# Performance work log

Measured on AMD Instinct MI355X. Metric: run time of the kernel, lower is better.

The kernel has to match this reference:

```python
import jax, jax.numpy as jnp
import numpy as np

B, C_IN, T = 8, 1024, 4096
D_VQ, K, DS = 1024, 2048, 2


def setup_inputs() -> dict:
    key = jax.random.key(0)
    k1, k2, k3, k4 = jax.random.split(key, 4)
    x = jax.random.normal(k1, (B, C_IN, T), dtype=jnp.float32)
    x_mask = jnp.ones((B, 1, T), dtype=jnp.float32)
    conv_in_w = jax.random.normal(k2, (D_VQ, C_IN, DS), dtype=jnp.float32) * 0.02
    conv_in_b = jnp.zeros((D_VQ,), dtype=jnp.float32)
    codebook = jax.random.normal(k3, (K, D_VQ), dtype=jnp.float32)
    conv_out_w = jax.random.normal(k4, (C_IN, D_VQ), dtype=jnp.float32) * 0.02
    conv_out_b = jnp.zeros((C_IN,), dtype=jnp.float32)
    return {"x": x, "x_mask": x_mask, "conv_in_w": conv_in_w,
            "conv_in_b": conv_in_b, "codebook": codebook,
            "conv_out_w": conv_out_w, "conv_out_b": conv_out_b}


def reference(x, x_mask, conv_in_w, conv_in_b, codebook, conv_out_w, conv_out_b):
    x_len = x.shape[2]  # 4096, divisible by DS=2 -> no padding branch
    # conv_in: Conv1d(C_IN -> D_VQ, kernel=DS, stride=DS)
    h = jax.lax.conv_general_dilated(
        x, conv_in_w, window_strides=(DS,), padding='VALID',
        dimension_numbers=('NCH', 'OIH', 'NCH')) + conv_in_b[None, :, None]
    xt = h.transpose(0, 2, 1)  # [B, T', D]
    # euclidean VQ: squared distances to codebook, argmin assignment
    d2 = (jnp.sum(xt * xt, -1, keepdims=True)
          - 2.0 * jnp.einsum('btd,kd->btk', xt, codebook)
          + jnp.sum(codebook * codebook, -1))  # [B, T', K]
    idx = jnp.argmin(d2, axis=-1)  # [B, T'] int
    quant = codebook[idx]  # [B, T', D]
    # commitment loss (EMA codebook: codebook detached)
    loss = jnp.mean(jnp.square(xt - jax.lax.stop_gradient(quant)))
    # straight-through estimator
    q = xt + jax.lax.stop_gradient(quant - xt)
    qc = q.transpose(0, 2, 1)  # [B, D, T']
    # conv_out: nearest upsample by DS, then 1x1 conv
    up = jnp.repeat(qc, DS, axis=-1)  # [B, D, T]
    out = jnp.einsum('od,bdt->bot', conv_out_w, up) + conv_out_b[None, :, None]
    out = (out * x_mask)[:, :, :x_len]
    indices = idx[:, None, :]  # 'b t -> b 1 t'
    return out, indices, loss
```

## Files before the change

kernel.cpp:

```cpp
#include <hip/hip_runtime.h>

#define NB   8
#define CIN  1024
#define TT   4096
#define DVQ  1024
#define KC   2048
#define MM   16384

typedef short s16x8 __attribute__((ext_vector_type(8)));
typedef float f32x4 __attribute__((ext_vector_type(4)));

__device__ __forceinline__ short f2bf(float f) {
    unsigned u = __float_as_uint(f);
    u = u + 0x7fffu + ((u >> 16) & 1u);
    return (short)(u >> 16);
}
__device__ __forceinline__ float bf2f(short h) {
    return __uint_as_float(((unsigned)(unsigned short)h) << 16);
}
__device__ __forceinline__ unsigned pk(short a, short b) {
    return (unsigned)(unsigned short)a | ((unsigned)(unsigned short)b << 16);
}
__device__ __forceinline__ void split3(float v, short& h, short& m, short& l) {
    h = f2bf(v); float r1 = v - bf2f(h);
    m = f2bf(r1); float r2 = r1 - bf2f(m);
    l = f2bf(r2);
}
__device__ __forceinline__ int aswz(int row, int q) {
    return row * 40 + (((q ^ (row >> 3)) & 3) << 3);
}
__device__ __forceinline__ bool lesskey(float v, int k, float v2, int k2) {
    return v < v2 || (v == v2 && k < k2);
}
__device__ __forceinline__ void merge2(float& b1, int& k1, float& b2, int& k2,
                                       float o1, int ok1, float o2, int ok2) {
    if (lesskey(o1, ok1, b1, k1)) {
        float nb2; int nk2;
        if (lesskey(b1, k1, o2, ok2)) { nb2 = b1; nk2 = k1; } else { nb2 = o2; nk2 = ok2; }
        b1 = o1; k1 = ok1; b2 = nb2; k2 = nk2;
    } else if (lesskey(o1, ok1, b2, k2)) {
        b2 = o1; k2 = ok1;
    }
}
__device__ __forceinline__ void gload16(void* lds, const void* g) {
    __builtin_amdgcn_global_load_lds((const __attribute__((address_space(1))) void*)g,
                                     (__attribute__((address_space(3))) void*)lds, 16, 0, 0);
}

__global__ __launch_bounds__(256) void k_split3(const float* __restrict__ src,
                                                short* __restrict__ h, short* __restrict__ m,
                                                short* __restrict__ l, int n4) {
    int i = blockIdx.x * 256 + threadIdx.x;
    if (i >= n4) return;
    float4 v = ((const float4*)src)[i];
    short4 H, M, L;
    split3(v.x, H.x, M.x, L.x); split3(v.y, H.y, M.y, L.y);
    split3(v.z, H.z, M.z, L.z); split3(v.w, H.w, M.w, L.w);
    ((short4*)h)[i] = H; ((short4*)m)[i] = M; ((short4*)l)[i] = L;
}

__global__ __launch_bounds__(256) void k_split2(const float* __restrict__ src,
                                                short* __restrict__ h, short* __restrict__ l, int n4) {
    int i = blockIdx.x * 256 + threadIdx.x;
    if (i >= n4) return;
    float4 v = ((const float4*)src)[i];
    short4 H, L;
    H.x = f2bf(v.x); L.x = f2bf(v.x - bf2f(H.x));
    H.y = f2bf(v.y); L.y = f2bf(v.y - bf2f(H.y));
    H.z = f2bf(v.z); L.z = f2bf(v.z - bf2f(H.z));
    H.w = f2bf(v.w); L.w = f2bf(v.w - bf2f(H.w));
    ((short4*)h)[i] = H; ((short4*)l)[i] = L;
}

__global__ __launch_bounds__(256) void k_cnorm(const float* __restrict__ cb,
                                               float* __restrict__ c32,
                                               double* __restrict__ c64) {
    __shared__ double red[256];
    const float* row = cb + (size_t)blockIdx.x * DVQ;
    float4 v = ((const float4*)row)[threadIdx.x];
    red[threadIdx.x] = (double)v.x * v.x + (double)v.y * v.y +
                       (double)v.z * v.z + (double)v.w * v.w;
    __syncthreads();
    for (int o = 128; o > 0; o >>= 1) {
        if (threadIdx.x < o) red[threadIdx.x] += red[threadIdx.x + o];
        __syncthreads();
    }
    if (threadIdx.x == 0) { c64[blockIdx.x] = red[0]; c32[blockIdx.x] = (float)red[0]; }
}

__global__ __launch_bounds__(256) void k_asplit(const float* __restrict__ x,
                                                short* __restrict__ ah,
                                                short* __restrict__ am,
                                                short* __restrict__ al) {
    const int bid = blockIdx.x;
    const int b = bid >> 7, cblk = (bid >> 5) & 3, tch = bid & 31;
    const int c = cblk * 256 + threadIdx.x;
    const float* xr = x + ((size_t)b * CIN + c) * TT + tch * 128;
    unsigned* AH = (unsigned*)ah;
    unsigned* AM = (unsigned*)am;
    unsigned* AL = (unsigned*)al;
    const int mbase = b * 2048 + tch * 64;
#pragma unroll 4
    for (int i = 0; i < 32; ++i) {
        float4 v = *(const float4*)(xr + 4 * i);
        short h0, mm0, l0, h1, mm1, l1, h2, mm2, l2, h3, mm3, l3;
        split3(v.x, h0, mm0, l0); split3(v.y, h1, mm1, l1);
        split3(v.z, h2, mm2, l2); split3(v.w, h3, mm3, l3);
        const size_t o0 = (size_t)(mbase + 2 * i) * 1024 + c;
        const size_t o1 = o0 + 1024;
        AH[o0] = pk(h0, h1); AM[o0] = pk(mm0, mm1); AL[o0] = pk(l0, l1);
        AH[o1] = pk(h2, h3); AM[o1] = pk(mm2, mm3); AL[o1] = pk(l2, l3);
    }
}

__global__ __launch_bounds__(512, 2) void k_convp(const short* __restrict__ ah,
                                                  const short* __restrict__ am,
                                                  const short* __restrict__ al,
                                                  const short* __restrict__ wh,
                                                  const short* __restrict__ wm,
                                                  const short* __restrict__ wl,
                                                  const float* __restrict__ bias,
                                                  float* __restrict__ xt,
                                                  short* __restrict__ xth,
                                                  short* __restrict__ xtl) {
    __shared__ short sA[2][3][256 * 32];
    __shared__ short sB[2][3][128 * 32];
    const int tid = threadIdx.x;
    const int lin = blockIdx.x;
    const int cx = lin & 7, j = lin >> 3;
    const int m0 = (cx * 8 + (j >> 3)) * 256;
    const int n0 = (j & 7) * 128;

    const int s0 = tid, s1 = tid + 512;
    const int ar0 = s0 >> 2, ac0 = ((s0 & 3) ^ ((s0 >> 3) & 3)) << 3;
    const int ar1 = s1 >> 2, ac1 = ((s1 & 3) ^ ((s1 >> 3) & 3)) << 3;
    const size_t gA0 = (size_t)(m0 + ar0) * 2048 + ac0;
    const size_t gA1 = (size_t)(m0 + ar1) * 2048 + ac1;
    const size_t gB0 = (size_t)(n0 + ar0) * 2048 + ac0;

    const int ln = tid & 15, quad = (tid >> 4) & 3, wv = tid >> 6;
    const int qsw = (quad ^ ((ln >> 1) & 3)) * 8;
    const int r0w = (wv >> 1) * 64, c0w = (wv & 1) * 64;

    f32x4 acc[4][4], sums[4][4];
#pragma unroll
    for (int r = 0; r < 4; ++r)
#pragma unroll
        for (int c = 0; c < 4; ++c) { acc[r][c] = 0.f; sums[r][c] = 0.f; }

#define STAGE(BUF, K0)                                        \
    do {                                                      \
        gload16(&sA[BUF][0][s0 * 8], ah + gA0 + (K0));        \
        gload16(&sA[BUF][0][s1 * 8], ah + gA1 + (K0));        \
        gload16(&sA[BUF][1][s0 * 8], am + gA0 + (K0));        \
        gload16(&sA[BUF][1][s1 * 8], am + gA1 + (K0));        \
        gload16(&sA[BUF][2][s0 * 8], al + gA0 + (K0));        \
        gload16(&sA[BUF][2][s1 * 8], al + gA1 + (K0));        \
        gload16(&sB[BUF][0][s0 * 8], wh + gB0 + (K0));        \
        gload16(&sB[BUF][1][s0 * 8], wm + gB0 + (K0));        \
        gload16(&sB[BUF][2][s0 * 8], wl + gB0 + (K0));        \
    } while (0)

    STAGE(0, 0);
    __syncthreads();

#pragma unroll 2
    for (int it = 0; it < 64; ++it) {
        const int cur = it & 1;
        if (it + 1 < 64) STAGE(cur ^ 1, (it + 1) * 32);

        s16x8 fa0[4], fa1[4], fa2[4];
#pragma unroll
        for (int r = 0; r < 4; ++r) {
            const int off = (r0w + r * 16 + ln) * 32 + qsw;
            fa0[r] = *(const s16x8*)&sA[cur][0][off];
            fa1[r] = *(const s16x8*)&sA[cur][1][off];
            fa2[r] = *(const s16x8*)&sA[cur][2][off];
        }
#pragma unroll
        for (int c = 0; c < 4; ++c) {
            const int boff = (c0w + c * 16 + ln) * 32 + qsw;
            s16x8 fbh = *(const s16x8*)&sB[cur][0][boff];
            s16x8 fbm = *(const s16x8*)&sB[cur][1][boff];
            s16x8 fbl = *(const s16x8*)&sB[cur][2][boff];
#pragma unroll
            for (int r = 0; r < 4; ++r) {
                acc[r][c] = __builtin_amdgcn_mfma_f32_16x16x32_bf16(fa0[r], fbh, acc[r][c], 0, 0, 0);
                acc[r][c] = __builtin_amdgcn_mfma_f32_16x16x32_bf16(fa0[r], fbm, acc[r][c], 0, 0, 0);
                acc[r][c] = __builtin_amdgcn_mfma_f32_16x16x32_bf16(fa1[r], fbh, acc[r][c], 0, 0, 0);
                acc[r][c] = __builtin_amdgcn_mfma_f32_16x16x32_bf16(fa0[r], fbl, acc[r][c], 0, 0, 0);
                acc[r][c] = __builtin_amdgcn_mfma_f32_16x16x32_bf16(fa1[r], fbm, acc[r][c], 0, 0, 0);
                acc[r][c] = __builtin_amdgcn_mfma_f32_16x16x32_bf16(fa2[r], fbh, acc[r][c], 0, 0, 0);
            }
        }
        if (it & 1) {
#pragma unroll
            for (int r = 0; r < 4; ++r)
#pragma unroll
                for (int c = 0; c < 4; ++c) { sums[r][c] += acc[r][c]; acc[r][c] = 0.f; }
        }
        __syncthreads();
    }
#undef STAGE
#pragma unroll
    for (int c = 0; c < 4; ++c) {
        const int n = n0 + c0w + c * 16 + ln;
        const float bv = bias[n];
#pragma unroll
        for (int r = 0; r < 4; ++r)
#pragma unroll
            for (int g = 0; g < 4; ++g) {
                const int m = m0 + r0w + r * 16 + quad * 4 + g;
                const float v = sums[r][c][g] + bv;
                const size_t o = (size_t)m * DVQ + n;
                xt[o] = v;
                short h = f2bf(v);
                xth[o] = h;
                xtl[o] = f2bf(v - bf2f(h));
            }
    }
}

__global__ __launch_bounds__(256, 2) void k_conv(const float* __restrict__ x,
                                                 const short* __restrict__ wh,
                                                 const short* __restrict__ wm,
                                                 const short* __restrict__ wl,
                                                 const float* __restrict__ bias,
                                                 float* __restrict__ xt,
                                                 short* __restrict__ xth,
                                                 short* __restrict__ xtl) {
    __shared__ short sAh[128 * 40], sAm[128 * 40], sAl[128 * 40];
    __shared__ short sBh[64 * 40],  sBm[64 * 40],  sBl[64 * 40];
    const int tid = threadIdx.x;
    const int lin = blockIdx.x;
    const int cx = lin & 7, j = lin >> 3;
    const int m0 = (cx * 16 + (j >> 4)) * 128;
    const int n0 = (j & 15) * 64;
    const int b = m0 >> 11, t0 = m0 & 2047;
    const float* xb = x + (size_t)b * CIN * TT + 2 * t0;

    const int aw = tid >> 6, p = tid & 63;
    const int brow = tid >> 2, bq = tid & 3;
    const int ln = tid & 15, quad = (tid >> 4) & 3;
    const int r0 = (aw >> 1) * 64, c0 = (aw & 1) * 32;

    f32x4 acc[4][2], sums[4][2];
#pragma unroll
    for (int r = 0; r < 4; ++r)
#pragma unroll
        for (int c = 0; c < 2; ++c) { acc[r][c] = 0.f; sums[r][c] = 0.f; }

    float4 av[4];
    uint4 bh0, bm0, bl0;
#pragma unroll
    for (int r = 0; r < 4; ++r) av[r] = *(const float4*)(xb + (size_t)(4 * r + aw) * TT + 4 * p);
    {
        const size_t o = (size_t)(n0 + brow) * 2048 + bq * 8;
        bh0 = *(const uint4*)&wh[o]; bm0 = *(const uint4*)&wm[o]; bl0 = *(const uint4*)&wl[o];
    }

    for (int it = 0; it < 64; ++it) {
        __syncthreads();
#pragma unroll
        for (int r = 0; r < 4; ++r) {
            const int ii = r * 4 + aw;
            const int q = ii >> 2, off = (2 * ii) & 7;
            const int a0 = aswz(2 * p, q) + off;
            const int a1 = aswz(2 * p + 1, q) + off;
            float4 v = av[r];
            short hx, mx, lx, hy, my, ly;
            split3(v.x, hx, mx, lx); split3(v.y, hy, my, ly);
            *(unsigned*)&sAh[a0] = pk(hx, hy);
            *(unsigned*)&sAm[a0] = pk(mx, my);
            *(unsigned*)&sAl[a0] = pk(lx, ly);
            split3(v.z, hx, mx, lx); split3(v.w, hy, my, ly);
            *(unsigned*)&sAh[a1] = pk(hx, hy);
            *(unsigned*)&sAm[a1] = pk(mx, my);
            *(unsigned*)&sAl[a1] = pk(lx, ly);
        }
        {
            const int w0 = brow * 40 + bq * 8;
            *(uint4*)&sBh[w0] = bh0; *(uint4*)&sBm[w0] = bm0; *(uint4*)&sBl[w0] = bl0;
        }
        __syncthreads();
        if (it + 1 < 64) {
            const int i0 = (it + 1) * 16, k0 = (it + 1) * 32;
#pragma unroll
            for (int r = 0; r < 4; ++r)
                av[r] = *(const float4*)(xb + (size_t)(i0 + 4 * r + aw) * TT + 4 * p);
            const size_t o = (size_t)(n0 + brow) * 2048 + k0 + bq * 8;
            bh0 = *(const uint4*)&wh[o]; bm0 = *(const uint4*)&wm[o]; bl0 = *(const uint4*)&wl[o];
        }
        s16x8 fah[4], fam[4], fal[4];
#pragma unroll
        for (int r = 0; r < 4; ++r) {
            const int base = aswz(r0 + r * 16 + ln, quad);
            fah[r] = *(const s16x8*)&sAh[base];
            fam[r] = *(const s16x8*)&sAm[base];
            fal[r] = *(const s16x8*)&sAl[base];
        }
#pragma unroll
        for (int c = 0; c < 2; ++c) {
            const int bb = (c0 + c * 16 + ln) * 40 + quad * 8;
            s16x8 fbh = *(const s16x8*)&sBh[bb];
            s16x8 fbm = *(const s16x8*)&sBm[bb];
            s16x8 fbl = *(const s16x8*)&sBl[bb];
#pragma unroll
            for (int r = 0; r < 4; ++r) {
                acc[r][c] = __builtin_amdgcn_mfma_f32_16x16x32_bf16(fah[r], fbh, acc[r][c], 0, 0, 0);
                acc[r][c] = __builtin_amdgcn_mfma_f32_16x16x32_bf16(fah[r], fbm, acc[r][c], 0, 0, 0);
                acc[r][c] = __builtin_amdgcn_mfma_f32_16x16x32_bf16(fam[r], fbh, acc[r][c], 0, 0, 0);
                acc[r][c] = __builtin_amdgcn_mfma_f32_16x16x32_bf16(fah[r], fbl, acc[r][c], 0, 0, 0);
                acc[r][c] = __builtin_amdgcn_mfma_f32_16x16x32_bf16(fam[r], fbm, acc[r][c], 0, 0, 0);
                acc[r][c] = __builtin_amdgcn_mfma_f32_16x16x32_bf16(fal[r], fbh, acc[r][c], 0, 0, 0);
            }
        }
        if (it & 1) {
#pragma unroll
            for (int r = 0; r < 4; ++r)
#pragma unroll
                for (int c = 0; c < 2; ++c) { sums[r][c] += acc[r][c]; acc[r][c] = 0.f; }
        }
    }
#pragma unroll
    for (int c = 0; c < 2; ++c) {
        const int n = n0 + c0 + c * 16 + ln;
        const float bv = bias[n];
#pragma unroll
        for (int r = 0; r < 4; ++r)
#pragma unroll
            for (int g = 0; g < 4; ++g) {
                const int m = m0 + r0 + r * 16 + quad * 4 + g;
                const float v = sums[r][c][g] + bv;
                const size_t o = (size_t)m * DVQ + n;
                xt[o] = v;
                short h = f2bf(v);
                xth[o] = h;
                xtl[o] = f2bf(v - bf2f(h));
            }
    }
}

__global__ __launch_bounds__(256, 2) void k_dot(const short* __restrict__ xth,
                                                const short* __restrict__ xtl,
                                                const short* __restrict__ cbh,
                                                const short* __restrict__ cbl,
                                                const float* __restrict__ c32,
                                                float4* __restrict__ pb) {
    __shared__ __align__(16) short sAh[128 * 40], sAl[128 * 40], sBh[128 * 40], sBl[128 * 40];
    const int tid = threadIdx.x;
    const int n0 = blockIdx.x * 128, m0 = blockIdx.y * 128;
    const int ar = tid >> 2, q = tid & 3, kk = q * 8;
    const int ln = tid & 15, quad = (tid >> 4) & 3, wv = tid >> 6;
    const int r0 = (wv >> 1) * 64, c0 = (wv & 1) * 64;

    f32x4 acc[4][4];
#pragma unroll
    for (int r = 0; r < 4; ++r)
#pragma unroll
        for (int c = 0; c < 4; ++c) acc[r][c] = 0.f;

    uint4 a0 = *(const uint4*)&xth[(size_t)(m0 + ar) * 1024 + kk];
    uint4 a1 = *(const uint4*)&xth[(size_t)(m0 + 64 + ar) * 1024 + kk];
    uint4 a2 = *(const uint4*)&xtl[(size_t)(m0 + ar) * 1024 + kk];
    uint4 a3 = *(const uint4*)&xtl[(size_t)(m0 + 64 + ar) * 1024 + kk];
    uint4 b0 = *(const uint4*)&cbh[(size_t)(n0 + ar) * 1024 + kk];
    uint4 b1 = *(const uint4*)&cbh[(size_t)(n0 + 64 + ar) * 1024 + kk];
    uint4 b2 = *(const uint4*)&cbl[(size_t)(n0 + ar) * 1024 + kk];
    uint4 b3 = *(const uint4*)&cbl[(size_t)(n0 + 64 + ar) * 1024 + kk];

    for (int it = 0; it < 32; ++it) {
        __syncthreads();
        *(uint4*)&sAh[aswz(ar, q)] = a0;
        *(uint4*)&sAh[aswz(64 + ar, q)] = a1;
        *(uint4*)&sAl[aswz(ar, q)] = a2;
        *(uint4*)&sAl[aswz(64 + ar, q)] = a3;
        {
            const int w0 = ar * 40 + kk, w1 = (64 + ar) * 40 + kk;
            *(uint4*)&sBh[w0] = b0; *(uint4*)&sBh[w1] = b1;
            *(uint4*)&sBl[w0] = b2; *(uint4*)&sBl[w1] = b3;
        }
        __syncthreads();
        if (it + 1 < 32) {
            const int k0 = (it + 1) * 32;
            a0 = *(const uint4*)&xth[(size_t)(m0 + ar) * 1024 + k0 + kk];
            a1 = *(const uint4*)&xth[(size_t)(m0 + 64 + ar) * 1024 + k0 + kk];
            a2 = *(const uint4*)&xtl[(size_t)(m0 + ar) * 1024 + k0 + kk];
            a3 = *(const uint4*)&xtl[(size_t)(m0 + 64 + ar) * 1024 + k0 + kk];
            b0 = *(const uint4*)&cbh[(size_t)(n0 + ar) * 1024 + k0 + kk];
            b1 = *(const uint4*)&cbh[(size_t)(n0 + 64 + ar) * 1024 + k0 + kk];
            b2 = *(const uint4*)&cbl[(size_t)(n0 + ar) * 1024 + k0 + kk];
            b3 = *(const uint4*)&cbl[(size_t)(n0 + 64 + ar) * 1024 + k0 + kk];
        }
        s16x8 fah[4], fal[4];
#pragma unroll
        for (int r = 0; r < 4; ++r) {
            const int base = aswz(r0 + r * 16 + ln, quad);
            fah[r] = *(const s16x8*)&sAh[base];
            fal[r] = *(const s16x8*)&sAl[base];
        }
#pragma unroll
        for (int c = 0; c < 4; ++c) {
            const int bb = (c0 + c * 16 + ln) * 40 + quad * 8;
            s16x8 fbh = *(const s16x8*)&sBh[bb];
            s16x8 fbl = *(const s16x8*)&sBl[bb];
#pragma unroll
            for (int r = 0; r < 4; ++r) {
                acc[r][c] = __builtin_amdgcn_mfma_f32_16x16x32_bf16(fah[r], fbh, acc[r][c], 0, 0, 0);
                acc[r][c] = __builtin_amdgcn_mfma_f32_16x16x32_bf16(fah[r], fbl, acc[r][c], 0, 0, 0);
                acc[r][c] = __builtin_amdgcn_mfma_f32_16x16x32_bf16(fal[r], fbh, acc[r][c], 0, 0, 0);
            }
        }
    }
    float tb1[16], tb2[16]; int tk1[16], tk2[16];
#pragma unroll
    for (int i = 0; i < 16; ++i) { tb1[i] = INFINITY; tb2[i] = INFINITY; tk1[i] = 0; tk2[i] = 0; }
#pragma unroll
    for (int c = 0; c < 4; ++c) {
        const int n = n0 + c0 + c * 16 + ln;
        const float cn = c32[n];
#pragma unroll
        for (int r = 0; r < 4; ++r)
#pragma unroll
            for (int g = 0; g < 4; ++g) {
                const float s = cn - 2.0f * acc[r][c][g];
                const int i = r * 4 + g;
                if (s < tb1[i]) { tb2[i] = tb1[i]; tk2[i] = tk1[i]; tb1[i] = s; tk1[i] = n; }
                else if (s < tb2[i]) { tb2[i] = s; tk2[i] = n; }
            }
    }
#pragma unroll
    for (int off = 1; off < 16; off <<= 1) {
#pragma unroll
        for (int i = 0; i < 16; ++i) {
            float o1 = __shfl_xor(tb1[i], off); int ok1 = __shfl_xor(tk1[i], off);
            float o2 = __shfl_xor(tb2[i], off); int ok2 = __shfl_xor(tk2[i], off);
            merge2(tb1[i], tk1[i], tb2[i], tk2[i], o1, ok1, o2, ok2);
        }
    }
    __syncthreads();
    float4* part = (float4*)sAh;
    if (ln == 0) {
#pragma unroll
        for (int i = 0; i < 16; ++i) {
            const int lr = (i >> 2) * 16 + quad * 4 + (i & 3);
            float4 v; v.x = tb1[i]; v.y = tb2[i];
            v.z = __int_as_float(tk1[i]); v.w = __int_as_float(tk2[i]);
            part[wv * 64 + lr] = v;
        }
    }
    __syncthreads();
    if (tid < 128) {
        const int row = tid, h = row >> 6, lr = row & 63;
        float4 A = part[(2 * h) * 64 + lr];
        float4 B = part[(2 * h + 1) * 64 + lr];
        float b1v = A.x, b2v = A.y; int k1 = __float_as_int(A.z), k2 = __float_as_int(A.w);
        merge2(b1v, k1, b2v, k2, B.x, __float_as_int(B.z), B.y, __float_as_int(B.w));
        float4 o; o.x = b1v; o.y = b2v; o.z = __int_as_float(k1); o.w = __int_as_float(k2);
        pb[(size_t)blockIdx.x * MM + m0 + row] = o;
    }
}

__global__ __launch_bounds__(256) void k_pick(const float4* __restrict__ pb,
                                              const double* __restrict__ c64,
                                              const float* __restrict__ xt,
                                              const float* __restrict__ cb,
                                              int* __restrict__ idxbuf,
                                              float* __restrict__ idx_out) {
    const int wv = threadIdx.x >> 6, lane = threadIdx.x & 63;
    const int m = blockIdx.x * 4 + wv;
    float4 P = pb[m];
    float b1 = P.x, b2 = P.y; int k1 = __float_as_int(P.z), k2 = __float_as_int(P.w);
#pragma unroll
    for (int s = 1; s < 16; ++s) {
        float4 Q = pb[(size_t)s * MM + m];
        merge2(b1, k1, b2, k2, Q.x, __float_as_int(Q.z), Q.y, __float_as_int(Q.w));
    }
    const float* xr = xt + (size_t)m * DVQ;
    const float* c1 = cb + (size_t)k1 * DVQ;
    const float* c2 = cb + (size_t)k2 * DVQ;
    double e1 = 0.0, e2 = 0.0;
    for (int j = 0; j < DVQ / 64; ++j) {
        const int d = j * 64 + lane;
        const double xv = xr[d];
        e1 += xv * (double)c1[d]; e2 += xv * (double)c2[d];
    }
    for (int off = 32; off > 0; off >>= 1) { e1 += __shfl_xor(e1, off); e2 += __shfl_xor(e2, off); }
    if (lane == 0) {
        const double s1 = c64[k1] - 2.0 * e1;
        const double s2 = c64[k2] - 2.0 * e2;
        const int kf = (s2 < s1 || (s2 == s1 && k2 < k1)) ? k2 : k1;
        idxbuf[m] = kf;
        idx_out[m] = (float)kf;
    }
}

__global__ __launch_bounds__(256) void k_losspart(const float* __restrict__ xt,
                                                  const float* __restrict__ cb,
                                                  const int* __restrict__ idxbuf,
                                                  float* __restrict__ partials) {
    __shared__ float red[256];
    const int m = blockIdx.x;
    const int row = idxbuf[m];
    float4 a = ((const float4*)(xt + (size_t)m * DVQ))[threadIdx.x];
    float4 c = ((const float4*)(cb + (size_t)row * DVQ))[threadIdx.x];
    const float dx = a.x - c.x, dy = a.y - c.y, dz = a.z - c.z, dw = a.w - c.w;
    red[threadIdx.x] = dx * dx + dy * dy + dz * dz + dw * dw;
    __syncthreads();
    for (int o = 128; o > 0; o >>= 1) {
        if (threadIdx.x < o) red[threadIdx.x] += red[threadIdx.x + o];
        __syncthreads();
    }
    if (threadIdx.x == 0) partials[m] = red[0];
}

__global__ __launch_bounds__(256) void k_lossfinal(const float* __restrict__ partials,
                                                   float* __restrict__ loss_out) {
    __shared__ float red[256];
    float s = 0.0f;
    for (int i = threadIdx.x; i < MM; i += 256) s += partials[i];
    red[threadIdx.x] = s;
    __syncthreads();
    for (int o = 128; o > 0; o >>= 1) {
        if (threadIdx.x < o) red[threadIdx.x] += red[threadIdx.x + o];
        __syncthreads();
    }
    if (threadIdx.x == 0) loss_out[0] = red[0] / (float)((size_t)MM * DVQ);
}

__global__ __launch_bounds__(256, 2) void k_out(const int* __restrict__ idxbuf,
                                                const short* __restrict__ ch,
                                                const short* __restrict__ cl,
                                                const short* __restrict__ wh,
                                                const short* __restrict__ wl,
                                                const float* __restrict__ bias,
                                                const float* __restrict__ xm,
                                                float* __restrict__ outp) {
    __shared__ short sAh[128 * 40], sAl[128 * 40], sBh[128 * 40], sBl[128 * 40];
    __shared__ int rows_s[128];
    const int tid = threadIdx.x;
    const int m0 = blockIdx.y * 128, n0 = blockIdx.x * 128;
    if (tid < 128) rows_s[tid] = idxbuf[m0 + tid];
    __syncthreads();
    const int ar = tid >> 2, q = tid & 3, kk = q * 8;
    const int ln = tid & 15, quad = (tid >> 4) & 3, wv = tid >> 6;
    const int r0 = (wv >> 1) * 64, c0 = (wv & 1) * 64;
    const size_t ra0 = (size_t)rows_s[ar] * 1024, ra1 = (size_t)rows_s[64 + ar] * 1024;

    f32x4 acc[4][4];
#pragma unroll
    for (int r = 0; r < 4; ++r)
#pragma unroll
        for (int c = 0; c < 4; ++c) acc[r][c] = 0.f;

    uint4 a0 = *(const uint4*)&ch[ra0 + kk];
    uint4 a1 = *(const uint4*)&ch[ra1 + kk];
    uint4 a2 = *(const uint4*)&cl[ra0 + kk];
    uint4 a3 = *(const uint4*)&cl[ra1 + kk];
    uint4 b0 = *(const uint4*)&wh[(size_t)(n0 + ar) * 1024 + kk];
    uint4 b1 = *(const uint4*)&wh[(size_t)(n0 + 64 + ar) * 1024 + kk];
    uint4 b2 = *(const uint4*)&wl[(size_t)(n0 + ar) * 1024 + kk];
    uint4 b3 = *(const uint4*)&wl[(size_t)(n0 + 64 + ar) * 1024 + kk];

    for (int it = 0; it < 32; ++it) {
        __syncthreads();
        *(uint4*)&sAh[aswz(ar, q)] = a0;
        *(uint4*)&sAh[aswz(64 + ar, q)] = a1;
        *(uint4*)&sAl[aswz(ar, q)] = a2;
        *(uint4*)&sAl[aswz(64 + ar, q)] = a3;
        {
            const int w0 = ar * 40 + kk, w1 = (64 + ar) * 40 + kk;
            *(uint4*)&sBh[w0] = b0; *(uint4*)&sBh[w1] = b1;
            *(uint4*)&sBl[w0] = b2; *(uint4*)&sBl[w1] = b3;
        }
        __syncthreads();
        if (it + 1 < 32) {
            const int k0 = (it + 1) * 32;
            a0 = *(const uint4*)&ch[ra0 + k0 + kk];
            a1 = *(const uint4*)&ch[ra1 + k0 + kk];
            a2 = *(const uint4*)&cl[ra0 + k0 + kk];
            a3 = *(const uint4*)&cl[ra1 + k0 + kk];
            b0 = *(const uint4*)&wh[(size_t)(n0 + ar) * 1024 + k0 + kk];
            b1 = *(const uint4*)&wh[(size_t)(n0 + 64 + ar) * 1024 + k0 + kk];
            b2 = *(const uint4*)&wl[(size_t)(n0 + ar) * 1024 + k0 + kk];
            b3 = *(const uint4*)&wl[(size_t)(n0 + 64 + ar) * 1024 + k0 + kk];
        }
        s16x8 fah[4], fal[4];
#pragma unroll
        for (int r = 0; r < 4; ++r) {
            const int base = aswz(r0 + r * 16 + ln, quad);
            fah[r] = *(const s16x8*)&sAh[base];
            fal[r] = *(const s16x8*)&sAl[base];
        }
#pragma unroll
        for (int c = 0; c < 4; ++c) {
            const int bb = (c0 + c * 16 + ln) * 40 + quad * 8;
            s16x8 fbh = *(const s16x8*)&sBh[bb];
            s16x8 fbl = *(const s16x8*)&sBl[bb];
#pragma unroll
            for (int r = 0; r < 4; ++r) {
                acc[r][c] = __builtin_amdgcn_mfma_f32_16x16x32_bf16(fah[r], fbh, acc[r][c], 0, 0, 0);
                acc[r][c] = __builtin_amdgcn_mfma_f32_16x16x32_bf16(fah[r], fbl, acc[r][c], 0, 0, 0);
                acc[r][c] = __builtin_amdgcn_mfma_f32_16x16x32_bf16(fal[r], fbh, acc[r][c], 0, 0, 0);
            }
        }
    }
#pragma unroll
    for (int c = 0; c < 4; ++c) {
        const int n = n0 + c0 + c * 16 + ln;
        const float bv = bias[n];
#pragma unroll
        for (int r = 0; r < 4; ++r)
#pragma unroll
            for (int g = 0; g < 4; ++g) {
                const int m = m0 + r0 + r * 16 + quad * 4 + g;
                const int b = m >> 11, t = m & 2047;
                const float mk0 = xm[(size_t)b * TT + 2 * t];
                const float mk1 = xm[(size_t)b * TT + 2 * t + 1];
                const float v = acc[r][c][g] + bv;
                float2 o2; o2.x = v * mk0; o2.y = v * mk1;
                *(float2*)&outp[((size_t)b * CIN + n) * TT + 2 * t] = o2;
            }
    }
}

extern "C" void kernel_launch(void* const* d_in, const int* in_sizes, int n_in,
                              void* d_out, int out_size, void* d_ws, size_t ws_size,
                              hipStream_t stream) {
    const float* x  = (const float*)d_in[0];
    const float* xm = (const float*)d_in[1];
    const float* wi = (const float*)d_in[2];
    const float* bi = (const float*)d_in[3];
    const float* cb = (const float*)d_in[4];
    const float* wo = (const float*)d_in[5];
    const float* bo = (const float*)d_in[6];

    float* outp     = (float*)d_out;
    float* idx_out  = outp + (size_t)NB * CIN * TT;
    float* loss_out = idx_out + MM;
    float* xt  = outp;
    short* xth = (short*)(outp + 16777216);
    short* xtl = xth + 16777216;

    char* p = (char*)d_ws;
    short* wih = (short*)p; p += (size_t)CIN * 2048 * 2;
    short* wim = (short*)p; p += (size_t)CIN * 2048 * 2;
    short* wil = (short*)p; p += (size_t)CIN * 2048 * 2;
    short* cbh = (short*)p; p += (size_t)KC * DVQ * 2;
    short* cbl = (short*)p; p += (size_t)KC * DVQ * 2;
    short* woh = (short*)p; p += (size_t)CIN * DVQ * 2;
    short* wol = (short*)p; p += (size_t)CIN * DVQ * 2;
    float*  c32 = (float*)p;  p += KC * sizeof(float);
    double* c64 = (double*)p; p += KC * sizeof(double);
    float4* pb  = (float4*)p; p += (size_t)16 * MM * sizeof(float4);
    float* partials = (float*)p; p += MM * sizeof(float);
    int*   idxbuf   = (int*)p;   p += MM * sizeof(int);
    short* Ah = (short*)p; p += (size_t)MM * 2048 * 2;
    short* Am = (short*)p; p += (size_t)MM * 2048 * 2;
    short* Al = (short*)p; p += (size_t)MM * 2048 * 2;
    const size_t need = (size_t)(p - (char*)d_ws);
    const bool fast = ws_size >= need;

    dim3 blk(256);
    k_split3<<<dim3(2048), blk, 0, stream>>>(wi, wih, wim, wil, CIN * 2048 / 4);
    k_split2<<<dim3(2048), blk, 0, stream>>>(cb, cbh, cbl, KC * DVQ / 4);
    k_split2<<<dim3(1024), blk, 0, stream>>>(wo, woh, wol, CIN * DVQ / 4);
    k_cnorm <<<dim3(KC),   blk, 0, stream>>>(cb, c32, c64);
    if (fast) {
        k_asplit<<<dim3(1024), blk, 0, stream>>>(x, Ah, Am, Al);
        k_convp <<<dim3(512), dim3(512), 0, stream>>>(Ah, Am, Al, wih, wim, wil, bi, xt, xth, xtl);
    } else {
        k_conv  <<<dim3(2048), blk, 0, stream>>>(x, wih, wim, wil, bi, xt, xth, xtl);
    }
    k_dot   <<<dim3(16, 128), blk, 0, stream>>>(xth, xtl, cbh, cbl, c32, pb);
    k_pick  <<<dim3(MM / 4), blk, 0, stream>>>(pb, c64, xt, cb, idxbuf, idx_out);
    k_losspart<<<dim3(MM), blk, 0, stream>>>(xt, cb, idxbuf, partials);
    k_lossfinal<<<1, blk, 0, stream>>>(partials, loss_out);
    k_out   <<<dim3(8, 128), blk, 0, stream>>>(idxbuf, cbh, cbl, woh, wol, bo, xm, outp);
}
```

Measured before the change: 1.099 ms.

## Software-pipeline conv_in GEMM main loop with phased barriers and setprio

Rewrites the double-buffered split-bf16 GEMM main loop so both stages are prefetched ahead and each K-tile runs as interleaved phases of LDS fragment reads and MFMA bursts. The phases are separated by explicit barriers and s_waitcnt vmcnt waits instead of a __syncthreads per iteration, and MFMA bursts are wrapped in s_setprio. The goal is to overlap global-to-LDS loads and LDS reads with matrix math and to keep waves in step. It adds many more barriers per tile and relies on hand-counted vmcnt values, which could stall or become unsafe if the load count changes.

```diff
diff --git a/kernel.cpp b/kernel.cpp
--- a/kernel.cpp
+++ b/kernel.cpp
@@ -46,6 +46,12 @@
     __builtin_amdgcn_global_load_lds((const __attribute__((address_space(1))) void*)g,
                                      (__attribute__((address_space(3))) void*)lds, 16, 0, 0);
 }
+#define WAITV(N) asm volatile("s_waitcnt vmcnt(" #N ")" ::: "memory")
+#define BARRIER() do { asm volatile("" ::: "memory"); \
+                       __builtin_amdgcn_s_barrier();  \
+                       asm volatile("" ::: "memory"); } while (0)
+#define SCHED0() __builtin_amdgcn_sched_barrier(0)
+#define PH_BAR() do { SCHED0(); BARRIER(); SCHED0(); } while (0)
 
 __global__ __launch_bounds__(256) void k_split3(const float* __restrict__ src,
                                                 short* __restrict__ h, short* __restrict__ m,
@@ -148,6 +154,10 @@
 #pragma unroll
         for (int c = 0; c < 4; ++c) { acc[r][c] = 0.f; sums[r][c] = 0.f; }
 
+    s16x8 fa0[4], fa1[4], fa2[4];
+    s16x8 feh, fem, fel;
+    s16x8 foh, fom, fol;
+
 #define STAGE(BUF, K0)                                        \
     do {                                                      \
         gload16(&sA[BUF][0][s0 * 8], ah + gA0 + (K0));        \
@@ -161,47 +171,96 @@
         gload16(&sB[BUF][2][s0 * 8], wl + gB0 + (K0));        \
     } while (0)
 
+#define RDA(CUR, r)                                           \
+    do {                                                      \
+        const int off_ = (r0w + (r) * 16 + ln) * 32 + qsw;    \
+        fa0[r] = *(const s16x8*)&sA[CUR][0][off_];            \
+        fa1[r] = *(const s16x8*)&sA[CUR][1][off_];            \
+        fa2[r] = *(const s16x8*)&sA[CUR][2][off_];            \
+    } while (0)
+#define RDBE(CUR, c)                                          \
+    do {                                                      \
+        const int boff_ = (c0w + (c) * 16 + ln) * 32 + qsw;   \
+        feh = *(const s16x8*)&sB[CUR][0][boff_];              \
+        fem = *(const s16x8*)&sB[CUR][1][boff_];              \
+        fel = *(const s16x8*)&sB[CUR][2][boff_];              \
+    } while (0)
+#define RDBO(CUR, c)                                          \
+    do {                                                      \
+        const int boff_ = (c0w + (c) * 16 + ln) * 32 + qsw;   \
+        foh = *(const s16x8*)&sB[CUR][0][boff_];              \
+        fom = *(const s16x8*)&sB[CUR][1][boff_];              \
+        fol = *(const s16x8*)&sB[CUR][2][boff_];              \
+    } while (0)
+#define MF6(r, c, H, M, L)                                                        \
+    do {                                                                          \
+        acc[r][c] = __builtin_amdgcn_mfma_f32_16x16x32_bf16(fa0[r], H, acc[r][c], 0, 0, 0); \
+        acc[r][c] = __builtin_amdgcn_mfma_f32_16x16x32_bf16(fa0[r], M, acc[r][c], 0, 0, 0); \
+        acc[r][c] = __builtin_amdgcn_mfma_f32_16x16x32_bf16(fa1[r], H, acc[r][c], 0, 0, 0); \
+        acc[r][c] = __builtin_amdgcn_mfma_f32_16x16x32_bf16(fa0[r], L, acc[r][c], 0, 0, 0); \
+        acc[r][c] = __builtin_amdgcn_mfma_f32_16x16x32_bf16(fa1[r], M, acc[r][c], 0, 0, 0); \
+        acc[r][c] = __builtin_amdgcn_mfma_f32_16x16x32_bf16(fa2[r], H, acc[r][c], 0, 0, 0); \
+    } while (0)
+#define FLUSH_                                                \
+    {                                                         \
+        _Pragma("unroll")                                     \
+        for (int r_ = 0; r_ < 4; ++r_)                        \
+            _Pragma("unroll")                                 \
+            for (int c_ = 0; c_ < 4; ++c_) {                  \
+                sums[r_][c_] += acc[r_][c_];                  \
+                acc[r_][c_] = 0.f;                            \
+            }                                                 \
+    }
+
+#define TILE(CUR, WAITSTMT, STAGESTMT, FLUSHSTMT)             \
+    do {                                                      \
+        WAITSTMT;                                             \
+        PH_BAR();                         \
+        RDA(CUR, 0); RDA(CUR, 1); RDBE(CUR, 0);               \
+        PH_BAR();                                             \
+        __builtin_amdgcn_s_setprio(1);                        \
+        MF6(0, 0, feh, fem, fel); MF6(1, 0, feh, fem, fel);   \
+        __builtin_amdgcn_s_setprio(0);                        \
+        RDA(CUR, 2); RDA(CUR, 3);                             \
+        PH_BAR();                                             \
+        __builtin_amdgcn_s_setprio(1);                        \
+        MF6(2, 0, feh, fem, fel); MF6(3, 0, feh, fem, fel);   \
+        __builtin_amdgcn_s_setprio(0);                        \
+        RDBO(CUR, 1);                                         \
+        PH_BAR();                                             \
+        __builtin_amdgcn_s_setprio(1);                        \
+        MF6(0, 1, foh, fom, fol); MF6(1, 1, foh, fom, fol);   \
+        MF6(2, 1, foh, fom, fol); MF6(3, 1, foh, fom, fol);   \
+        __builtin_amdgcn_s_setprio(0);                        \
+        RDBE(CUR, 2);                                         \
+        PH_BAR();                                             \
+        __builtin_amdgcn_s_setprio(1);                        \
+        MF6(0, 2, feh, fem, fel); MF6(1, 2, feh, fem, fel);   \
+        MF6(2, 2, feh, fem, fel); MF6(3, 2, feh, fem, fel);   \
+        __builtin_amdgcn_s_setprio(0);                        \
+        RDBO(CUR, 3);                                         \
+        PH_BAR();                                             \
+        __builtin_amdgcn_s_setprio(1);                        \
+        MF6(0, 3, foh, fom, fol); MF6(1, 3, foh, fom, fol);   \
+        MF6(2, 3, foh, fom, fol); MF6(3, 3, foh, fom, fol);   \
+        __builtin_amdgcn_s_setprio(0);                        \
+        FLUSHSTMT;                                            \
+        PH_BAR();                         \
+        STAGESTMT;                                            \
+    } while (0)
+
     STAGE(0, 0);
-    __syncthreads();
-
-#pragma unroll 2
-    for (int it = 0; it < 64; ++it) {
-        const int cur = it & 1;
-        if (it + 1 < 64) STAGE(cur ^ 1, (it + 1) * 32);
-
-        s16x8 fa0[4], fa1[4], fa2[4];
-#pragma unroll
-        for (int r = 0; r < 4; ++r) {
-            const int off = (r0w + r * 16 + ln) * 32 + qsw;
-            fa0[r] = *(const s16x8*)&sA[cur][0][off];
-            fa1[r] = *(const s16x8*)&sA[cur][1][off];
-            fa2[r] = *(const s16x8*)&sA[cur][2][off];
-        }
-#pragma unroll
-        for (int c = 0; c < 4; ++c) {
-            const int boff = (c0w + c * 16 + ln) * 32 + qsw;
-            s16x8 fbh = *(const s16x8*)&sB[cur][0][boff];
-            s16x8 fbm = *(const s16x8*)&sB[cur][1][boff];
-            s16x8 fbl = *(const s16x8*)&sB[cur][2][boff];
-#pragma unroll
-            for (int r = 0; r < 4; ++r) {
-                acc[r][c] = __builtin_amdgcn_mfma_f32_16x16x32_bf16(fa0[r], fbh, acc[r][c], 0, 0, 0);
-                acc[r][c] = __builtin_amdgcn_mfma_f32_16x16x32_bf16(fa0[r], fbm, acc[r][c], 0, 0, 0);
-                acc[r][c] = __builtin_amdgcn_mfma_f32_16x16x32_bf16(fa1[r], fbh, acc[r][c], 0, 0, 0);
-                acc[r][c] = __builtin_amdgcn_mfma_f32_16x16x32_bf16(fa0[r], fbl, acc[r][c], 0, 0, 0);
-                acc[r][c] = __builtin_amdgcn_mfma_f32_16x16x32_bf16(fa1[r], fbm, acc[r][c], 0, 0, 0);
-                acc[r][c] = __builtin_amdgcn_mfma_f32_16x16x32_bf16(fa2[r], fbh, acc[r][c], 0, 0, 0);
-            }
-        }
-        if (it & 1) {
-#pragma unroll
-            for (int r = 0; r < 4; ++r)
-#pragma unroll
-                for (int c = 0; c < 4; ++c) { sums[r][c] += acc[r][c]; acc[r][c] = 0.f; }
-        }
-        __syncthreads();
-    }
+    STAGE(1, 32);
+
+    for (int ii = 0; ii < 31; ++ii) {
+        TILE(0, WAITV(9), STAGE(0, (2 * ii + 2) * 32), (void)0);
+        TILE(1, WAITV(9), STAGE(1, (2 * ii + 3) * 32), FLUSH_);
+    }
+    TILE(0, WAITV(9), (void)0, (void)0);
+    TILE(1, WAITV(0), (void)0, FLUSH_);
+#undef TILE
 #undef STAGE
+
 #pragma unroll
     for (int c = 0; c < 4; ++c) {
         const int n = n0 + c0w + c * 16 + ln;
```

After: 1.102 ms. Within noise of the previous version (+0.2%).
